# Performance work log

Hardware: AMD Instinct MI355X
Metric: run time of the kernel (lower is better)

Reference implementation:

```python
import jax, jax.numpy as jnp
import numpy as np

# pywt 'db4' analysis filters (dec_lo, dec_hi)
DEC_LO = np.array([-0.010597401784997278, 0.032883011666982945, 0.030841381835986965,
                   -0.18703481171888114, -0.02798376941698385, 0.6308807679295904,
                   0.7148465705525415, 0.23037781330885523], dtype=np.float32)
DEC_HI = np.array([-0.23037781330885523, 0.7148465705525415, -0.6308807679295904,
                   -0.02798376941698385, 0.18703481171888114, 0.030841381835986965,
                   -0.032883011666982945, -0.010597401784997278], dtype=np.float32)
J = 3          # dwt levels for subwindow_size=64 with db4
DWT_LEN = 84   # 14 (lo) + 35 + 21 + 14 (his)
NEG_SLOPE = 1e-3
FILT = np.stack([DEC_LO[::-1].copy(), DEC_HI[::-1].copy()])[:, None, :]  # [2,1,8] reversed, as in pytorch_wavelets


def _afb1d(x):
    # Single-level analysis filter bank along last axis, reflect padding (pytorch_wavelets mode='reflect')
    N = x.shape[-1]
    L = 8
    outsize = (N + L - 1) // 2
    p = 2 * (outsize - 1) - N + L
    xp = jnp.pad(x, [(0, 0)] * (x.ndim - 1) + [(p // 2, (p + 1) // 2)], mode='reflect')
    lead = x.shape[:-1]
    xr = xp.reshape((-1, 1, xp.shape[-1]))
    out = jax.lax.conv_general_dilated(xr, jnp.asarray(FILT, dtype=x.dtype), (2,), 'VALID')  # [B,2,outsize]
    lo = out[:, 0].reshape(lead + (outsize,))
    hi = out[:, 1].reshape(lead + (outsize,))
    return lo, hi


def _dwt(x):
    # J-level DWT; returns concat([lo_J, hi_1, ..., hi_J], axis=-1), matching [x_lo]+x_hi cat order
    his = []
    lo = x
    for _ in range(J):
        lo, hi = _afb1d(lo)
        his.append(hi)
    return jnp.concatenate([lo] + his, axis=-1)


def setup_inputs() -> dict:
    key = jax.random.key(0)
    k1, k2, k3 = jax.random.split(key, 3)
    B, K = 16384, 16
    x = jax.random.normal(k1, (B, 1, 64, 8, 8), dtype=jnp.float32)
    conv_w = jax.random.normal(k2, (K, 1, DWT_LEN, 8, 8), dtype=jnp.float32) * (1.0 / np.sqrt(DWT_LEN * 64))
    conv_b = jax.random.normal(k3, (K,), dtype=jnp.float32) * 0.01
    return {"x": x, "conv_w": conv_w, "conv_b": conv_b}


def reference(x, conv_w, conv_b):
    # x: [B,1,T=64,8,8]; time_interval=1, no maxpool, subwindow_nbins=1 (subwindow = full window)
    xt = jnp.moveaxis(x, 2, -1)            # [B,1,8,8,T] -> DWT along time
    d = _dwt(xt)                           # [B,1,8,8,DWT_LEN]
    d = jnp.moveaxis(d, -1, 2)             # [B,1,DWT_LEN,8,8]
    # Conv3d with kernel spanning full [DWT_LEN,8,8] == full contraction -> [B,K]
    feat = jnp.einsum('bcdhw,kcdhw->bk', d, conv_w) + conv_b
    # Dropout3d is identity in eval; LeakyReLU(0.001) then flatten (already [B, nbins*K], nbins=1)
    return jnp.where(feat >= 0, feat, NEG_SLOPE * feat)
```

## Files before the change

### kernel.cpp

```cpp
#include <hip/hip_runtime.h>
#include <hip/hip_bf16.h>

#define DWT_LEN_C 84
#define TDIM 64
#define INNER 4096
#define KOUT 16
#define HCOLS 2048
#define OITER 16

typedef __attribute__((ext_vector_type(8))) short short8;
typedef __attribute__((ext_vector_type(4))) float floatx4;

__device__ __forceinline__ unsigned short bf16_rne(float f) {
    unsigned u = __float_as_uint(f);
    unsigned r = u + 0x7fffu + ((u >> 16) & 1u);
    return (unsigned short)(r >> 16);
}

__device__ const float c_dec_lo[8] = {-0.010597401784997278f, 0.032883011666982945f, 0.030841381835986965f,
                                      -0.18703481171888114f, -0.02798376941698385f, 0.6308807679295904f,
                                      0.7148465705525415f, 0.23037781330885523f};
__device__ const float c_dec_hi[8] = {-0.23037781330885523f, 0.7148465705525415f, -0.6308807679295904f,
                                      -0.02798376941698385f, 0.18703481171888114f, 0.030841381835986965f,
                                      -0.032883011666982945f, -0.010597401784997278f};

__device__ void afb1d_col(const float* v, int N, float* lo, float* hi, int M) {
    for (int i = 0; i < M; ++i) {
        float slo = 0.f, shi = 0.f;
        for (int j = 0; j < 8; ++j) {
            int idx = 2 * i + j - 6;
            if (idx < 0) idx = -idx;
            if (idx >= N) idx = 2 * N - 2 - idx;
            float c = v[idx];
            slo = fmaf(c, c_dec_lo[7 - j], slo);
            shi = fmaf(c, c_dec_hi[7 - j], shi);
        }
        lo[i] = slo; hi[i] = shi;
    }
}

__global__ __launch_bounds__(256) void build_weff_bf16(const float* __restrict__ conv_w,
                                                       unsigned short* __restrict__ Wb) {
    __shared__ float Wd[DWT_LEN_C][TDIM];
    const int t0 = threadIdx.x;
    if (t0 < TDIM) {
        float v[64];
        for (int n = 0; n < 64; ++n) v[n] = (n == t0) ? 1.f : 0.f;
        float lo1[35], hi1[35], lo2[21], hi2[21], lo3[14], hi3[14];
        afb1d_col(v, 64, lo1, hi1, 35);
        afb1d_col(lo1, 35, lo2, hi2, 21);
        afb1d_col(lo2, 21, lo3, hi3, 14);
        for (int i = 0; i < 14; ++i) Wd[i][t0] = lo3[i];
        for (int i = 0; i < 35; ++i) Wd[14 + i][t0] = hi1[i];
        for (int i = 0; i < 21; ++i) Wd[49 + i][t0] = hi2[i];
        for (int i = 0; i < 14; ++i) Wd[70 + i][t0] = hi3[i];
    }
    __syncthreads();

    const int idx = blockIdx.x * 256 + threadIdx.x;
    const int k = idx >> 12;
    const int col = idx & 4095;
    const int t = col >> 6;
    const int hw = col & 63;
    float s = 0.f;
    const float* cw = conv_w + (size_t)k * DWT_LEN_C * 64 + hw;
#pragma unroll 4
    for (int dd = 0; dd < DWT_LEN_C; ++dd)
        s = fmaf(cw[dd * 64], Wd[dd][t], s);
    Wb[idx] = bf16_rne(s);
}

__global__ __launch_bounds__(512, 2) void dwt_mfma_fused(const float* __restrict__ x,
                                                         const unsigned short* __restrict__ Wb,
                                                         const float* __restrict__ bias,
                                                         float* __restrict__ out, int B) {
    __shared__ __align__(16) unsigned short Wlds[2][KOUT * HCOLS];
    const int t = threadIdx.x;
    const int rowgroup = blockIdx.x;

    {
        const int half = t >> 8;
        const int u = t & 255;
        const int n = u & 15;
        const int c0 = (u >> 4) * 128;
        const unsigned short* src = Wb + n * INNER + half * HCOLS + c0;
#pragma unroll
        for (int g = 0; g < 16; ++g) {
            const int c = c0 + g * 8;
            *(short8*)&Wlds[half][n * HCOLS + (c ^ ((n & 7) * 8))] = *(const short8*)(src + g * 8);
        }
    }
    __syncthreads();

    const int lane = t & 63;
    const int wid = t >> 6;
    const int kh = wid >> 2;
    const int w4 = wid & 3;
    const int qg = lane >> 4;
    const int mrow = lane & 15;
    const int rowbase = rowgroup * 64 + w4 * 16;
    const float* xrow = x + (size_t)(rowbase + mrow) * INNER + kh * HCOLS + qg * 8;
    const unsigned short* wrow = &Wlds[kh][mrow * HCOLS];
    const int swz = (mrow & 7) * 8;

    floatx4 acc = {0.f, 0.f, 0.f, 0.f};
    float4 bufA[8], bufB[8];

#define XLOAD(buf, it)                                                          \
    {                                                                           \
        const float* p = xrow + (it) * 128;                                     \
        _Pragma("unroll")                                                       \
        for (int s = 0; s < 4; ++s) {                                           \
            buf[2 * s]     = *(const float4*)(p + s * 32);                      \
            buf[2 * s + 1] = *(const float4*)(p + s * 32 + 4);                  \
        }                                                                       \
    }

#define XCOMPUTE(buf, it)                                                       \
    {                                                                           \
        _Pragma("unroll")                                                       \
        for (int s = 0; s < 4; ++s) {                                           \
            const float4 lo = buf[2 * s];                                       \
            const float4 hi = buf[2 * s + 1];                                   \
            short8 a;                                                           \
            a[0] = (short)bf16_rne(lo.x); a[1] = (short)bf16_rne(lo.y);         \
            a[2] = (short)bf16_rne(lo.z); a[3] = (short)bf16_rne(lo.w);         \
            a[4] = (short)bf16_rne(hi.x); a[5] = (short)bf16_rne(hi.y);         \
            a[6] = (short)bf16_rne(hi.z); a[7] = (short)bf16_rne(hi.w);         \
            const int col = (it) * 128 + s * 32 + qg * 8;                       \
            const short8 b = *(const short8*)(wrow + (col ^ swz));              \
            acc = __builtin_amdgcn_mfma_f32_16x16x32_bf16(a, b, acc, 0, 0, 0);  \
        }                                                                       \
    }

    XLOAD(bufA, 0);
#pragma unroll 1
    for (int it = 0; it < OITER; it += 2) {
        XLOAD(bufB, it + 1);
        XCOMPUTE(bufA, it);
        if (it + 2 < OITER) XLOAD(bufA, it + 2);
        XCOMPUTE(bufB, it + 1);
    }
#undef XLOAD
#undef XCOMPUTE

    __syncthreads();
    float* red = (float*)&Wlds[0][0];
    if (kh == 1)
        *(float4*)&red[(w4 * 64 + lane) * 4] = *(float4*)&acc;
    __syncthreads();
    if (kh == 0) {
        const float4 o = *(const float4*)&red[(w4 * 64 + lane) * 4];
        acc[0] += o.x; acc[1] += o.y; acc[2] += o.z; acc[3] += o.w;
        const float bv = bias[mrow];
        const int orow = rowbase + qg * 4;
#pragma unroll
        for (int r = 0; r < 4; ++r) {
            float val = acc[r] + bv;
            val = (val >= 0.f) ? val : 1e-3f * val;
            out[(size_t)(orow + r) * KOUT + mrow] = val;
        }
    }
}

extern "C" void kernel_launch(void* const* d_in, const int* in_sizes, int n_in,
                              void* d_out, int out_size, void* d_ws, size_t ws_size,
                              hipStream_t stream) {
    const float* x      = (const float*)d_in[0];
    const float* conv_w = (const float*)d_in[1];
    const float* conv_b = (const float*)d_in[2];
    float* out = (float*)d_out;
    const int B = in_sizes[0] / INNER;

    unsigned short* Wb = (unsigned short*)d_ws;

    build_weff_bf16<<<(KOUT * INNER) / 256, 256, 0, stream>>>(conv_w, Wb);
    dwt_mfma_fused<<<B / 64, 512, 0, stream>>>(x, Wb, conv_b, out, B);
}
```

Before: 63.55 us.

## Stream W into LDS in double-buffered quarters with smaller 256-thread blocks

Replaces the one-time staging of the full 128KB bf16 weight matrix into LDS with a double-buffered scheme. Each block stages 1024-column quarters (64KB total LDS) while it computes on the previous quarter. Blocks shrink to 256 threads covering 32 rows, and the two waves per tile split each quarter in halves. The goal is to hide the weight-staging latency and raise occupancy by cutting LDS use. In exchange it adds barriers per quarter, shortens the per-wave prefetch depth on x, and doubles the number of blocks that each restage the weights.

```diff
diff --git a/kernel.cpp b/kernel.cpp
--- a/kernel.cpp
+++ b/kernel.cpp
@@ -5,8 +5,8 @@
 #define TDIM 64
 #define INNER 4096
 #define KOUT 16
-#define HCOLS 2048
-#define OITER 16
+#define QCOLS 1024
+#define ROWS_PB 32
 
 typedef __attribute__((ext_vector_type(8))) short short8;
 typedef __attribute__((ext_vector_type(4))) float floatx4;
@@ -70,45 +70,45 @@
     Wb[idx] = bf16_rne(s);
 }
 
-__global__ __launch_bounds__(512, 2) void dwt_mfma_fused(const float* __restrict__ x,
+__global__ __launch_bounds__(256, 2) void dwt_mfma_fused(const float* __restrict__ x,
                                                          const unsigned short* __restrict__ Wb,
                                                          const float* __restrict__ bias,
                                                          float* __restrict__ out, int B) {
-    __shared__ __align__(16) unsigned short Wlds[2][KOUT * HCOLS];
+    __shared__ __align__(16) unsigned short Wlds[2][KOUT * QCOLS];
     const int t = threadIdx.x;
     const int rowgroup = blockIdx.x;
 
-    {
-        const int half = t >> 8;
-        const int u = t & 255;
-        const int n = u & 15;
-        const int c0 = (u >> 4) * 128;
-        const unsigned short* src = Wb + n * INNER + half * HCOLS + c0;
-#pragma unroll
-        for (int g = 0; g < 16; ++g) {
-            const int c = c0 + g * 8;
-            *(short8*)&Wlds[half][n * HCOLS + (c ^ ((n & 7) * 8))] = *(const short8*)(src + g * 8);
-        }
+#define WSTAGE(b, q)                                                            \
+    {                                                                           \
+        const int n = t & 15;                                                   \
+        const int c0 = (t >> 4) * 64;                                           \
+        const unsigned short* src = Wb + n * INNER + (q) * QCOLS + c0;          \
+        _Pragma("unroll")                                                       \
+        for (int g = 0; g < 8; ++g) {                                           \
+            const int c = c0 + g * 8;                                           \
+            *(short8*)&Wlds[b][n * QCOLS + (c ^ ((n & 7) * 8))] =               \
+                *(const short8*)(src + g * 8);                                  \
+        }                                                                       \
     }
-    __syncthreads();
+
+    WSTAGE(0, 0);
 
     const int lane = t & 63;
     const int wid = t >> 6;
-    const int kh = wid >> 2;
-    const int w4 = wid & 3;
+    const int tile = wid >> 1;
+    const int h = wid & 1;
     const int qg = lane >> 4;
     const int mrow = lane & 15;
-    const int rowbase = rowgroup * 64 + w4 * 16;
-    const float* xrow = x + (size_t)(rowbase + mrow) * INNER + kh * HCOLS + qg * 8;
-    const unsigned short* wrow = &Wlds[kh][mrow * HCOLS];
+    const int rowbase = rowgroup * ROWS_PB + tile * 16;
+    const float* xrow = x + (size_t)(rowbase + mrow) * INNER + h * 512 + qg * 8;
     const int swz = (mrow & 7) * 8;
 
     floatx4 acc = {0.f, 0.f, 0.f, 0.f};
     float4 bufA[8], bufB[8];
 
-#define XLOAD(buf, it)                                                          \
+#define XLOAD(buf, q, it)                                                       \
     {                                                                           \
-        const float* p = xrow + (it) * 128;                                     \
+        const float* p = xrow + (q) * QCOLS + (it) * 128;                       \
         _Pragma("unroll")                                                       \
         for (int s = 0; s < 4; ++s) {                                           \
             buf[2 * s]     = *(const float4*)(p + s * 32);                      \
@@ -116,8 +116,9 @@
         }                                                                       \
     }
 
-#define XCOMPUTE(buf, it)                                                       \
+#define XCOMPUTE(buf, b, it)                                                    \
     {                                                                           \
+        const unsigned short* wrow = &Wlds[b][mrow * QCOLS];                    \
         _Pragma("unroll")                                                       \
         for (int s = 0; s < 4; ++s) {                                           \
             const float4 lo = buf[2 * s];                                       \
@@ -127,30 +128,38 @@
             a[2] = (short)bf16_rne(lo.z); a[3] = (short)bf16_rne(lo.w);         \
             a[4] = (short)bf16_rne(hi.x); a[5] = (short)bf16_rne(hi.y);         \
             a[6] = (short)bf16_rne(hi.z); a[7] = (short)bf16_rne(hi.w);         \
-            const int col = (it) * 128 + s * 32 + qg * 8;                       \
-            const short8 b = *(const short8*)(wrow + (col ^ swz));              \
-            acc = __builtin_amdgcn_mfma_f32_16x16x32_bf16(a, b, acc, 0, 0, 0);  \
+            const int col = h * 512 + (it) * 128 + s * 32 + qg * 8;             \
+            const short8 b2 = *(const short8*)(wrow + (col ^ swz));             \
+            acc = __builtin_amdgcn_mfma_f32_16x16x32_bf16(a, b2, acc, 0, 0, 0); \
         }                                                                       \
     }
 
-    XLOAD(bufA, 0);
+    __syncthreads();
+
 #pragma unroll 1
-    for (int it = 0; it < OITER; it += 2) {
-        XLOAD(bufB, it + 1);
-        XCOMPUTE(bufA, it);
-        if (it + 2 < OITER) XLOAD(bufA, it + 2);
-        XCOMPUTE(bufB, it + 1);
+    for (int q = 0; q < 4; ++q) {
+        const int cur = q & 1;
+        if (q < 3) WSTAGE(cur ^ 1, q + 1);
+        XLOAD(bufA, q, 0);
+        XLOAD(bufB, q, 1);
+        XCOMPUTE(bufA, cur, 0);
+        XLOAD(bufA, q, 2);
+        XCOMPUTE(bufB, cur, 1);
+        XLOAD(bufB, q, 3);
+        XCOMPUTE(bufA, cur, 2);
+        XCOMPUTE(bufB, cur, 3);
+        __syncthreads();
     }
+#undef WSTAGE
 #undef XLOAD
 #undef XCOMPUTE
 
+    float* red = (float*)&Wlds[0][0];
+    if (h == 1)
+        *(float4*)&red[(tile * 64 + lane) * 4] = *(float4*)&acc;
     __syncthreads();
-    float* red = (float*)&Wlds[0][0];
-    if (kh == 1)
-        *(float4*)&red[(w4 * 64 + lane) * 4] = *(float4*)&acc;
-    __syncthreads();
-    if (kh == 0) {
-        const float4 o = *(const float4*)&red[(w4 * 64 + lane) * 4];
+    if (h == 0) {
+        const float4 o = *(const float4*)&red[(tile * 64 + lane) * 4];
         acc[0] += o.x; acc[1] += o.y; acc[2] += o.z; acc[3] += o.w;
         const float bv = bias[mrow];
         const int orow = rowbase + qg * 4;
@@ -175,5 +184,5 @@
     unsigned short* Wb = (unsigned short*)d_ws;
 
     build_weff_bf16<<<(KOUT * INNER) / 256, 256, 0, stream>>>(conv_w, Wb);
-    dwt_mfma_fused<<<B / 64, 512, 0, stream>>>(x, Wb, conv_b, out, B);
+    dwt_mfma_fused<<<B / ROWS_PB, 256, 0, stream>>>(x, Wb, conv_b, out, B);
 }
```

Result: slower. 69.44 us (+9.3%).
